# Kernel optimization log

Measured on AMD Instinct MI355X. Metric: run time of the kernel, lower is better.

The kernel has to match this reference:

```python
import jax, jax.numpy as jnp
import numpy as np

B, S, D, H = 4, 2048, 1024, 16
HD = D // H
MASKED_BIAS = -10000.0

def setup_inputs() -> dict:
    key = jax.random.key(0)
    ks = jax.random.split(key, 10)
    s = 0.02
    return {
        "hidden_states": jax.random.normal(ks[0], (B, S, D), dtype=jnp.float32),
        "Wq": jax.random.normal(ks[1], (D, D), dtype=jnp.float32) * s,
        "bq": jax.random.normal(ks[2], (D,), dtype=jnp.float32) * s,
        "Wk": jax.random.normal(ks[3], (D, D), dtype=jnp.float32) * s,
        "bk": jax.random.normal(ks[4], (D,), dtype=jnp.float32) * s,
        "Wv": jax.random.normal(ks[5], (D, D), dtype=jnp.float32) * s,
        "bv": jax.random.normal(ks[6], (D,), dtype=jnp.float32) * s,
        "Wo": jax.random.normal(ks[7], (D, D), dtype=jnp.float32) * s,
        "bo": jax.random.normal(ks[8], (D,), dtype=jnp.float32) * s,
        "comp": jnp.zeros((D,), dtype=jnp.float32),
    }

def reference(hidden_states, Wq, bq, Wk, bk, Wv, bv, Wo, bo, comp):
    x = hidden_states
    # torch Linear: y = x @ W.T + b
    q = (x @ Wq.T + bq).reshape(B, S, H, HD).transpose(0, 2, 1, 3)  # [B,H,S,hd]
    k = (x @ Wk.T + bk).reshape(B, S, H, HD).transpose(0, 2, 1, 3)
    v = (x @ Wv.T + bv).reshape(B, S, H, HD).transpose(0, 2, 1, 3)
    scores = jnp.einsum('bhqd,bhkd->bhqk', q, k) / jnp.sqrt(jnp.asarray(HD, dtype=q.dtype))
    causal = jnp.tril(jnp.ones((S, S), dtype=bool))  # [S,S]
    scores = jnp.where(causal[None, None], scores, jnp.asarray(MASKED_BIAS, dtype=scores.dtype))
    attn = jax.nn.softmax(scores, axis=-1)  # dropout p=0 (eval)
    out = jnp.einsum('bhqk,bhkd->bhqd', attn, v)  # [B,H,S,hd]
    out = out.transpose(0, 2, 1, 3).reshape(B, S, D)
    out = out @ Wo.T + bo
    out = out + comp[None, None, :]
    return out
```

## Files before the change

### kernel.cpp

```cpp
#include <hip/hip_runtime.h>
#include <hip/hip_bf16.h>

#define NB 4
#define NS 2048
#define ND 1024
#define NH 16
#define NHD 64
#define NM (NB*NS)

typedef __bf16 bf16_t;
typedef bf16_t bf8  __attribute__((ext_vector_type(8)));
typedef bf16_t bf4v __attribute__((ext_vector_type(4)));
typedef float  f4   __attribute__((ext_vector_type(4)));

#define GLDS16(g, l) __builtin_amdgcn_global_load_lds( \
    (const __attribute__((address_space(1))) void*)(g), \
    (__attribute__((address_space(3))) void*)(l), 16, 0, 0)

__global__ __launch_bounds__(256) void cvt_all(const float* __restrict__ x,
                                               const float* __restrict__ wq,
                                               const float* __restrict__ wk,
                                               const float* __restrict__ wv,
                                               const float* __restrict__ wo,
                                               bf16_t* __restrict__ Xb,
                                               bf16_t* __restrict__ Wqkv,
                                               bf16_t* __restrict__ Wob) {
    const int i = blockIdx.x * 256 + threadIdx.x;
    const float* src;
    bf16_t* dst;
    int off;
    if (i < 2097152) {
        src = x; dst = Xb; off = i;
    } else {
        const int j = i - 2097152;
        const int w = j >> 18;
        off = j & 262143;
        src = (w == 0 ? wq : w == 1 ? wk : w == 2 ? wv : wo);
        dst = (w == 3 ? Wob : Wqkv + ((size_t)w << 20));
    }
    const float4 v = ((const float4*)src)[off];
    bf4v o;
    o[0] = (bf16_t)v.x; o[1] = (bf16_t)v.y; o[2] = (bf16_t)v.z; o[3] = (bf16_t)v.w;
    ((bf4v*)dst)[off] = o;
}

__global__ __launch_bounds__(256) void gemm_qkv(const bf16_t* __restrict__ A,
                                                const bf16_t* __restrict__ Bw,
                                                const float* __restrict__ bq,
                                                const float* __restrict__ bk,
                                                const float* __restrict__ bv,
                                                bf16_t* __restrict__ Qh,
                                                bf16_t* __restrict__ Kh,
                                                bf16_t* __restrict__ Vh) {
    __shared__ __align__(16) bf16_t As[128 * 32];
    __shared__ __align__(16) bf16_t Bs[128 * 32];
    const int t = threadIdx.x;
    const int wave = t >> 6, lane = t & 63, ln = lane & 15, quad = lane >> 4;
    const int wm = (wave >> 1) * 64, wn = (wave & 1) * 64;
    const int nwg = gridDim.x * gridDim.y;
    int flat = blockIdx.y * gridDim.x + blockIdx.x;
    flat = (flat & 7) * (nwg >> 3) + (flat >> 3);
    const int m0 = (flat / gridDim.x) * 128, n0 = (flat % gridDim.x) * 128;
    const int K = 1024;

    f4 acc[4][4];
    const f4 z = {0.f, 0.f, 0.f, 0.f};
#pragma unroll
    for (int i = 0; i < 4; ++i)
#pragma unroll
        for (int j = 0; j < 4; ++j) acc[i][j] = z;

    const int srow = wave * 16 + (lane >> 2);
    const int scol = (lane & 3) * 8;
    const bf16_t* Ag0 = A  + (size_t)(m0 + srow) * K + scol;
    const bf16_t* Ag1 = A  + (size_t)(m0 + srow + 64) * K + scol;
    const bf16_t* Bg0 = Bw + (size_t)(n0 + srow) * K + scol;
    const bf16_t* Bg1 = Bw + (size_t)(n0 + srow + 64) * K + scol;
    bf16_t* Al0 = &As[srow * 32 + scol];
    bf16_t* Al1 = &As[(srow + 64) * 32 + scol];
    bf16_t* Bl0 = &Bs[srow * 32 + scol];
    bf16_t* Bl1 = &Bs[(srow + 64) * 32 + scol];

    for (int k0 = 0; k0 < K; k0 += 32) {
        __syncthreads();
        GLDS16(Ag0 + k0, Al0);
        GLDS16(Ag1 + k0, Al1);
        GLDS16(Bg0 + k0, Bl0);
        GLDS16(Bg1 + k0, Bl1);
        __syncthreads();
        bf8 af[4], bfr[4];
#pragma unroll
        for (int mt = 0; mt < 4; ++mt) af[mt]  = *(const bf8*)(&As[(wm + mt * 16 + ln) * 32 + quad * 8]);
#pragma unroll
        for (int nt = 0; nt < 4; ++nt) bfr[nt] = *(const bf8*)(&Bs[(wn + nt * 16 + ln) * 32 + quad * 8]);
#pragma unroll
        for (int mt = 0; mt < 4; ++mt)
#pragma unroll
            for (int nt = 0; nt < 4; ++nt)
                acc[mt][nt] = __builtin_amdgcn_mfma_f32_16x16x32_bf16(bfr[nt], af[mt], acc[mt][nt], 0, 0, 0);
    }

#pragma unroll
    for (int nt = 0; nt < 4; ++nt) {
        const int gn = n0 + wn + nt * 16 + quad * 4;
        const int sec = gn >> 10, nn = gn & 1023;
        const int hh = nn >> 6, d = nn & 63;
        const float4 b4 = *(const float4*)((sec == 0 ? bq : sec == 1 ? bk : bv) + nn);
        bf16_t* dstBase = (sec == 0 ? Qh : (sec == 1 ? Kh : Vh));
#pragma unroll
        for (int mt = 0; mt < 4; ++mt) {
            const int gm = m0 + wm + mt * 16 + ln;
            const int b = gm >> 11, s = gm & 2047;
            bf4v pk;
            pk[0] = (bf16_t)(acc[mt][nt][0] + b4.x);
            pk[1] = (bf16_t)(acc[mt][nt][1] + b4.y);
            pk[2] = (bf16_t)(acc[mt][nt][2] + b4.z);
            pk[3] = (bf16_t)(acc[mt][nt][3] + b4.w);
            *(bf4v*)(&dstBase[((size_t)(b * NH + hh) * NS + s) * NHD + d]) = pk;
        }
    }
}

__global__ __launch_bounds__(256) void attn_kernel(const bf16_t* __restrict__ Q,
                                                   const bf16_t* __restrict__ K,
                                                   const bf16_t* __restrict__ V,
                                                   bf16_t* __restrict__ O) {
    __shared__ __align__(16) bf16_t Ks[64 * 72];
    __shared__ __align__(16) bf16_t Vt[64 * 72];
    __shared__ __align__(16) bf16_t Ps[4][16 * 72];
    const int L = blockIdx.x;
    const int mm = L >> 3;
    const int h  = ((mm >> 5) << 3) | (L & 7);
    const int qt = 31 - (mm & 31);
    const int q0 = qt * 64;
    const int jmax = qt;
    const size_t head_off = (size_t)h * NS * NHD;
    const int t = threadIdx.x;
    const int wave = t >> 6, lane = t & 63, ln = lane & 15, quad = lane >> 4;

    const bf16_t* Qrow = Q + head_off + (size_t)(q0 + wave * 16 + ln) * NHD;
    bf8 qf0 = *(const bf8*)(Qrow + quad * 8);
    bf8 qf1 = *(const bf8*)(Qrow + 32 + quad * 8);
#pragma unroll
    for (int e = 0; e < 8; ++e) {
        qf0[e] = (bf16_t)((float)qf0[e] * 0.125f);
        qf1[e] = (bf16_t)((float)qf1[e] * 0.125f);
    }

    const bf16_t* Kg = K + head_off;
    const bf16_t* Vg = V + head_off;
    const int krow0 = t >> 3, kcol = (t & 7) * 8;

    uint4 kr0 = *(const uint4*)(Kg + (size_t)krow0 * NHD + kcol);
    uint4 kr1 = *(const uint4*)(Kg + (size_t)(krow0 + 32) * NHD + kcol);
    bf8  vr0 = *(const bf8*)(Vg + (size_t)lane * NHD + wave * 8);
    bf8  vr1 = *(const bf8*)(Vg + (size_t)lane * NHD + (wave + 4) * 8);
    *(uint4*)(&Ks[krow0 * 72 + kcol])        = kr0;
    *(uint4*)(&Ks[(krow0 + 32) * 72 + kcol]) = kr1;
#pragma unroll
    for (int e = 0; e < 8; ++e) {
        Vt[(wave * 8 + e) * 72 + lane]       = vr0[e];
        Vt[((wave + 4) * 8 + e) * 72 + lane] = vr1[e];
    }
    __syncthreads();

    f4 o[4];
    const f4 z = {0.f, 0.f, 0.f, 0.f};
#pragma unroll
    for (int i = 0; i < 4; ++i) o[i] = z;
    float ls = 0.f;

    bf16_t* Pw = &Ps[wave][0];

#pragma unroll 1
    for (int j = 0; j <= jmax; ++j) {
        if (j < jmax) {
            const size_t nb = (size_t)(j + 1) * 64;
            kr0 = *(const uint4*)(Kg + (nb + krow0) * NHD + kcol);
            kr1 = *(const uint4*)(Kg + (nb + krow0 + 32) * NHD + kcol);
            vr0 = *(const bf8*)(Vg + (nb + lane) * NHD + wave * 8);
            vr1 = *(const bf8*)(Vg + (nb + lane) * NHD + (wave + 4) * 8);
        }

        f4 s[4];
        __builtin_amdgcn_s_setprio(1);
#pragma unroll
        for (int nt = 0; nt < 4; ++nt) {
            const bf8 kf0 = *(const bf8*)(&Ks[(nt * 16 + ln) * 72 + quad * 8]);
            const bf8 kf1 = *(const bf8*)(&Ks[(nt * 16 + ln) * 72 + 32 + quad * 8]);
            s[nt] = z;
            s[nt] = __builtin_amdgcn_mfma_f32_16x16x32_bf16(kf0, qf0, s[nt], 0, 0, 0);
            s[nt] = __builtin_amdgcn_mfma_f32_16x16x32_bf16(kf1, qf1, s[nt], 0, 0, 0);
        }
        __builtin_amdgcn_s_setprio(0);

        if (j == jmax) {
            const int kv0 = j * 64;
            const int rowq = q0 + wave * 16 + ln;
#pragma unroll
            for (int nt = 0; nt < 4; ++nt) {
#pragma unroll
                for (int r = 0; r < 4; ++r)
                    if (kv0 + nt * 16 + quad * 4 + r > rowq) s[nt][r] = -1e30f;
            }
        }

#pragma unroll
        for (int nt = 0; nt < 4; ++nt)
#pragma unroll
            for (int r = 0; r < 4; ++r) {
                const float p = __expf(s[nt][r]);
                s[nt][r] = p;
                ls += p;
            }

#pragma unroll
        for (int nt = 0; nt < 4; ++nt) {
            bf4v pk;
#pragma unroll
            for (int r = 0; r < 4; ++r) pk[r] = (bf16_t)s[nt][r];
            *(bf4v*)(&Pw[ln * 72 + nt * 16 + quad * 4]) = pk;
        }
        asm volatile("s_waitcnt lgkmcnt(0)" ::: "memory");
        __builtin_amdgcn_sched_barrier(0);
        const bf8 p0 = *(const bf8*)(&Pw[ln * 72 + quad * 8]);
        const bf8 p1 = *(const bf8*)(&Pw[ln * 72 + 32 + quad * 8]);

        __builtin_amdgcn_s_setprio(1);
#pragma unroll
        for (int dt = 0; dt < 4; ++dt) {
            const bf8 v0 = *(const bf8*)(&Vt[(dt * 16 + ln) * 72 + quad * 8]);
            const bf8 v1 = *(const bf8*)(&Vt[(dt * 16 + ln) * 72 + 32 + quad * 8]);
            o[dt] = __builtin_amdgcn_mfma_f32_16x16x32_bf16(p0, v0, o[dt], 0, 0, 0);
            o[dt] = __builtin_amdgcn_mfma_f32_16x16x32_bf16(p1, v1, o[dt], 0, 0, 0);
        }
        __builtin_amdgcn_s_setprio(0);

        if (j < jmax) {
            __syncthreads();
            *(uint4*)(&Ks[krow0 * 72 + kcol])        = kr0;
            *(uint4*)(&Ks[(krow0 + 32) * 72 + kcol]) = kr1;
#pragma unroll
            for (int e = 0; e < 8; ++e) {
                Vt[(wave * 8 + e) * 72 + lane]       = vr0[e];
                Vt[((wave + 4) * 8 + e) * 72 + lane] = vr1[e];
            }
            __syncthreads();
        }
    }

    ls += __shfl_xor(ls, 16);
    ls += __shfl_xor(ls, 32);

    const int b = h >> 4, hh = h & 15;
#pragma unroll
    for (int r = 0; r < 4; ++r) {
        const float inv = 1.f / __shfl(ls, quad * 4 + r);
        const int gs = q0 + wave * 16 + quad * 4 + r;
#pragma unroll
        for (int dt = 0; dt < 4; ++dt)
            O[((size_t)(b * NS + gs)) * ND + hh * NHD + dt * 16 + ln] = (bf16_t)(o[dt][r] * inv);
    }
}

__global__ __launch_bounds__(256) void gemm_proj(const bf16_t* __restrict__ A,
                                                 const bf16_t* __restrict__ Bw,
                                                 const float* __restrict__ bo,
                                                 const float* __restrict__ comp,
                                                 float* __restrict__ out) {
    __shared__ __align__(16) bf16_t As[128 * 32];
    __shared__ __align__(16) bf16_t Bs[128 * 32];
    const int t = threadIdx.x;
    const int wave = t >> 6, lane = t & 63, ln = lane & 15, quad = lane >> 4;
    const int wm = (wave >> 1) * 64, wn = (wave & 1) * 64;
    const int nwg = gridDim.x * gridDim.y;
    int flat = blockIdx.y * gridDim.x + blockIdx.x;
    flat = (flat & 7) * (nwg >> 3) + (flat >> 3);
    const int m0 = (flat / gridDim.x) * 128, n0 = (flat % gridDim.x) * 128;
    const int K = 1024;

    f4 acc[4][4];
    const f4 z = {0.f, 0.f, 0.f, 0.f};
#pragma unroll
    for (int i = 0; i < 4; ++i)
#pragma unroll
        for (int j = 0; j < 4; ++j) acc[i][j] = z;

    const int srow = wave * 16 + (lane >> 2);
    const int scol = (lane & 3) * 8;
    const bf16_t* Ag0 = A  + (size_t)(m0 + srow) * K + scol;
    const bf16_t* Ag1 = A  + (size_t)(m0 + srow + 64) * K + scol;
    const bf16_t* Bg0 = Bw + (size_t)(n0 + srow) * K + scol;
    const bf16_t* Bg1 = Bw + (size_t)(n0 + srow + 64) * K + scol;
    bf16_t* Al0 = &As[srow * 32 + scol];
    bf16_t* Al1 = &As[(srow + 64) * 32 + scol];
    bf16_t* Bl0 = &Bs[srow * 32 + scol];
    bf16_t* Bl1 = &Bs[(srow + 64) * 32 + scol];

    for (int k0 = 0; k0 < K; k0 += 32) {
        __syncthreads();
        GLDS16(Ag0 + k0, Al0);
        GLDS16(Ag1 + k0, Al1);
        GLDS16(Bg0 + k0, Bl0);
        GLDS16(Bg1 + k0, Bl1);
        __syncthreads();
        bf8 af[4], bfr[4];
#pragma unroll
        for (int mt = 0; mt < 4; ++mt) af[mt]  = *(const bf8*)(&As[(wm + mt * 16 + ln) * 32 + quad * 8]);
#pragma unroll
        for (int nt = 0; nt < 4; ++nt) bfr[nt] = *(const bf8*)(&Bs[(wn + nt * 16 + ln) * 32 + quad * 8]);
#pragma unroll
        for (int mt = 0; mt < 4; ++mt)
#pragma unroll
            for (int nt = 0; nt < 4; ++nt)
                acc[mt][nt] = __builtin_amdgcn_mfma_f32_16x16x32_bf16(bfr[nt], af[mt], acc[mt][nt], 0, 0, 0);
    }

#pragma unroll
    for (int nt = 0; nt < 4; ++nt) {
        const int gn = n0 + wn + nt * 16 + quad * 4;
        const float4 b4 = *(const float4*)(bo + gn);
        const float4 c4 = *(const float4*)(comp + gn);
#pragma unroll
        for (int mt = 0; mt < 4; ++mt) {
            const int gm = m0 + wm + mt * 16 + ln;
            float4 v;
            v.x = acc[mt][nt][0] + b4.x + c4.x;
            v.y = acc[mt][nt][1] + b4.y + c4.y;
            v.z = acc[mt][nt][2] + b4.z + c4.z;
            v.w = acc[mt][nt][3] + b4.w + c4.w;
            *(float4*)(&out[(size_t)gm * ND + gn]) = v;
        }
    }
}

extern "C" void kernel_launch(void* const* d_in, const int* in_sizes, int n_in,
                              void* d_out, int out_size, void* d_ws, size_t ws_size,
                              hipStream_t stream) {
    const float* x    = (const float*)d_in[0];
    const float* Wq   = (const float*)d_in[1];
    const float* bq   = (const float*)d_in[2];
    const float* Wk   = (const float*)d_in[3];
    const float* bk   = (const float*)d_in[4];
    const float* Wv   = (const float*)d_in[5];
    const float* bv   = (const float*)d_in[6];
    const float* Wo   = (const float*)d_in[7];
    const float* bo   = (const float*)d_in[8];
    const float* comp = (const float*)d_in[9];
    float* out = (float*)d_out;

    char* w = (char*)d_ws;
    bf16_t* Xb   = (bf16_t*)(w);
    bf16_t* Wqkv = (bf16_t*)(w + 16777216);
    bf16_t* Wob  = (bf16_t*)(w + 23068672);
    bf16_t* Qh   = (bf16_t*)(w + 25165824);
    bf16_t* Kh   = (bf16_t*)(w + 41943040);
    bf16_t* Vh   = (bf16_t*)(w + 58720256);
    bf16_t* AOb  = (bf16_t*)(w + 75497472);

    cvt_all<<<12288, 256, 0, stream>>>(x, Wq, Wk, Wv, Wo, Xb, Wqkv, Wob);
    gemm_qkv<<<dim3(3072 / 128, NM / 128), 256, 0, stream>>>(Xb, Wqkv, bq, bk, bv, Qh, Kh, Vh);
    attn_kernel<<<2048, 256, 0, stream>>>(Qh, Kh, Vh, AOb);
    gemm_proj<<<dim3(1024 / 128, NM / 128), 256, 0, stream>>>(AOb, Wob, bo, comp, out);
}
```

Baseline: 283.9 us.

## Write V transposed from QKV GEMM so attention loads V tiles vectorised

The QKV GEMM epilogue now writes V in a per-head transposed layout [b,h,d,s] by swapping the MFMA operand order, so each lane holds consecutive sequence positions. The attention kernel can then copy V tiles into LDS with 16-byte stores instead of a scalar per-element transpose. In exchange, the Q and K epilogue writes become scalar 2-byte stores, and the workgroup swizzle for L2 locality in the GEMM is removed.

```diff
diff --git a/kernel.cpp b/kernel.cpp
--- a/kernel.cpp
+++ b/kernel.cpp
@@ -51,16 +51,13 @@
                                                 const float* __restrict__ bv,
                                                 bf16_t* __restrict__ Qh,
                                                 bf16_t* __restrict__ Kh,
-                                                bf16_t* __restrict__ Vh) {
+                                                bf16_t* __restrict__ VTh) {
     __shared__ __align__(16) bf16_t As[128 * 32];
     __shared__ __align__(16) bf16_t Bs[128 * 32];
     const int t = threadIdx.x;
     const int wave = t >> 6, lane = t & 63, ln = lane & 15, quad = lane >> 4;
     const int wm = (wave >> 1) * 64, wn = (wave & 1) * 64;
-    const int nwg = gridDim.x * gridDim.y;
-    int flat = blockIdx.y * gridDim.x + blockIdx.x;
-    flat = (flat & 7) * (nwg >> 3) + (flat >> 3);
-    const int m0 = (flat / gridDim.x) * 128, n0 = (flat % gridDim.x) * 128;
+    const int m0 = blockIdx.y * 128, n0 = blockIdx.x * 128;
     const int K = 1024;
 
     f4 acc[4][4];
@@ -97,33 +94,44 @@
         for (int mt = 0; mt < 4; ++mt)
 #pragma unroll
             for (int nt = 0; nt < 4; ++nt)
-                acc[mt][nt] = __builtin_amdgcn_mfma_f32_16x16x32_bf16(bfr[nt], af[mt], acc[mt][nt], 0, 0, 0);
-    }
-
+                acc[mt][nt] = __builtin_amdgcn_mfma_f32_16x16x32_bf16(af[mt], bfr[nt], acc[mt][nt], 0, 0, 0);
+    }
+
+    const int sec = n0 >> 10;
 #pragma unroll
     for (int nt = 0; nt < 4; ++nt) {
-        const int gn = n0 + wn + nt * 16 + quad * 4;
-        const int sec = gn >> 10, nn = gn & 1023;
+        const int gn = n0 + wn + nt * 16 + ln;
+        const int nn = gn & 1023;
         const int hh = nn >> 6, d = nn & 63;
-        const float4 b4 = *(const float4*)((sec == 0 ? bq : sec == 1 ? bk : bv) + nn);
-        bf16_t* dstBase = (sec == 0 ? Qh : (sec == 1 ? Kh : Vh));
-#pragma unroll
-        for (int mt = 0; mt < 4; ++mt) {
-            const int gm = m0 + wm + mt * 16 + ln;
-            const int b = gm >> 11, s = gm & 2047;
-            bf4v pk;
-            pk[0] = (bf16_t)(acc[mt][nt][0] + b4.x);
-            pk[1] = (bf16_t)(acc[mt][nt][1] + b4.y);
-            pk[2] = (bf16_t)(acc[mt][nt][2] + b4.z);
-            pk[3] = (bf16_t)(acc[mt][nt][3] + b4.w);
-            *(bf4v*)(&dstBase[((size_t)(b * NH + hh) * NS + s) * NHD + d]) = pk;
+        const float bias = (sec == 0 ? bq[nn] : (sec == 1 ? bk[nn] : bv[nn]));
+        if (sec < 2) {
+            bf16_t* dstBase = (sec == 0 ? Qh : Kh);
+#pragma unroll
+            for (int mt = 0; mt < 4; ++mt) {
+#pragma unroll
+                for (int r = 0; r < 4; ++r) {
+                    const int gm = m0 + wm + mt * 16 + quad * 4 + r;
+                    const int b = gm >> 11, s = gm & 2047;
+                    dstBase[((size_t)(b * NH + hh) * NS + s) * NHD + d] = (bf16_t)(acc[mt][nt][r] + bias);
+                }
+            }
+        } else {
+#pragma unroll
+            for (int mt = 0; mt < 4; ++mt) {
+                const int gm0 = m0 + wm + mt * 16 + quad * 4;
+                const int b = gm0 >> 11, s = gm0 & 2047;
+                bf4v pk;
+#pragma unroll
+                for (int r = 0; r < 4; ++r) pk[r] = (bf16_t)(acc[mt][nt][r] + bias);
+                *(bf4v*)(&VTh[((size_t)(b * NH + hh) * NHD + d) * NS + s]) = pk;
+            }
         }
     }
 }
 
 __global__ __launch_bounds__(256) void attn_kernel(const bf16_t* __restrict__ Q,
                                                    const bf16_t* __restrict__ K,
-                                                   const bf16_t* __restrict__ V,
+                                                   const bf16_t* __restrict__ VT,
                                                    bf16_t* __restrict__ O) {
     __shared__ __align__(16) bf16_t Ks[64 * 72];
     __shared__ __align__(16) bf16_t Vt[64 * 72];
@@ -147,21 +155,18 @@
         qf1[e] = (bf16_t)((float)qf1[e] * 0.125f);
     }
 
-    const bf16_t* Kg = K + head_off;
-    const bf16_t* Vg = V + head_off;
+    const bf16_t* Kg  = K  + head_off;
+    const bf16_t* VTg = VT + head_off;
     const int krow0 = t >> 3, kcol = (t & 7) * 8;
 
     uint4 kr0 = *(const uint4*)(Kg + (size_t)krow0 * NHD + kcol);
     uint4 kr1 = *(const uint4*)(Kg + (size_t)(krow0 + 32) * NHD + kcol);
-    bf8  vr0 = *(const bf8*)(Vg + (size_t)lane * NHD + wave * 8);
-    bf8  vr1 = *(const bf8*)(Vg + (size_t)lane * NHD + (wave + 4) * 8);
+    uint4 vr0 = *(const uint4*)(VTg + (size_t)krow0 * NS + kcol);
+    uint4 vr1 = *(const uint4*)(VTg + (size_t)(krow0 + 32) * NS + kcol);
     *(uint4*)(&Ks[krow0 * 72 + kcol])        = kr0;
     *(uint4*)(&Ks[(krow0 + 32) * 72 + kcol]) = kr1;
-#pragma unroll
-    for (int e = 0; e < 8; ++e) {
-        Vt[(wave * 8 + e) * 72 + lane]       = vr0[e];
-        Vt[((wave + 4) * 8 + e) * 72 + lane] = vr1[e];
-    }
+    *(uint4*)(&Vt[krow0 * 72 + kcol])        = vr0;
+    *(uint4*)(&Vt[(krow0 + 32) * 72 + kcol]) = vr1;
     __syncthreads();
 
     f4 o[4];
@@ -178,8 +183,8 @@
             const size_t nb = (size_t)(j + 1) * 64;
             kr0 = *(const uint4*)(Kg + (nb + krow0) * NHD + kcol);
             kr1 = *(const uint4*)(Kg + (nb + krow0 + 32) * NHD + kcol);
-            vr0 = *(const bf8*)(Vg + (nb + lane) * NHD + wave * 8);
-            vr1 = *(const bf8*)(Vg + (nb + lane) * NHD + (wave + 4) * 8);
+            vr0 = *(const uint4*)(VTg + (size_t)krow0 * NS + nb + kcol);
+            vr1 = *(const uint4*)(VTg + (size_t)(krow0 + 32) * NS + nb + kcol);
         }
 
         f4 s[4];
@@ -240,11 +245,8 @@
             __syncthreads();
             *(uint4*)(&Ks[krow0 * 72 + kcol])        = kr0;
             *(uint4*)(&Ks[(krow0 + 32) * 72 + kcol]) = kr1;
-#pragma unroll
-            for (int e = 0; e < 8; ++e) {
-                Vt[(wave * 8 + e) * 72 + lane]       = vr0[e];
-                Vt[((wave + 4) * 8 + e) * 72 + lane] = vr1[e];
-            }
+            *(uint4*)(&Vt[krow0 * 72 + kcol])        = vr0;
+            *(uint4*)(&Vt[(krow0 + 32) * 72 + kcol]) = vr1;
             __syncthreads();
         }
     }
@@ -355,11 +357,11 @@
     bf16_t* Wob  = (bf16_t*)(w + 23068672);
     bf16_t* Qh   = (bf16_t*)(w + 25165824);
     bf16_t* Kh   = (bf16_t*)(w + 41943040);
-    bf16_t* Vh   = (bf16_t*)(w + 58720256);
+    bf16_t* VTh  = (bf16_t*)(w + 58720256);
     bf16_t* AOb  = (bf16_t*)(w + 75497472);
 
     cvt_all<<<12288, 256, 0, stream>>>(x, Wq, Wk, Wv, Wo, Xb, Wqkv, Wob);
-    gemm_qkv<<<dim3(3072 / 128, NM / 128), 256, 0, stream>>>(Xb, Wqkv, bq, bk, bv, Qh, Kh, Vh);
-    attn_kernel<<<2048, 256, 0, stream>>>(Qh, Kh, Vh, AOb);
+    gemm_qkv<<<dim3(3072 / 128, NM / 128), 256, 0, stream>>>(Xb, Wqkv, bq, bk, bv, Qh, Kh, VTh);
+    attn_kernel<<<2048, 256, 0, stream>>>(Qh, Kh, VTh, AOb);
     gemm_proj<<<dim3(1024 / 128, NM / 128), 256, 0, stream>>>(AOb, Wob, bo, comp, out);
 }
```

Measured after the change: 280.1 us. Within noise of the previous version (-1.3%).
